# Kernel optimization log

Hardware: AMD Instinct MI355X
Metric: run time of the kernel (lower is better)

The kernel has to match this reference:

```python
import jax, jax.numpy as jnp
import numpy as np
from jax import lax

NMS_THRESH = 0.5
BN_EPS = 1e-5
TO_REMOVE = 1.0  # neural-motifs box convention (+1 in width/height)


def nms_overlaps(boxes):
    # boxes: [N, C, 4] xyxy -> per-class pairwise IoU [N, N, C]
    x1 = jnp.maximum(boxes[:, None, :, 0], boxes[None, :, :, 0])
    y1 = jnp.maximum(boxes[:, None, :, 1], boxes[None, :, :, 1])
    x2 = jnp.minimum(boxes[:, None, :, 2], boxes[None, :, :, 2])
    y2 = jnp.minimum(boxes[:, None, :, 3], boxes[None, :, :, 3])
    inter = jnp.clip(x2 - x1 + TO_REMOVE, 0.0) * jnp.clip(y2 - y1 + TO_REMOVE, 0.0)
    area = (boxes[:, :, 2] - boxes[:, :, 0] + TO_REMOVE) * (boxes[:, :, 3] - boxes[:, :, 1] + TO_REMOVE)  # [N,C]
    union = area[:, None, :] + area[None, :, :] - inter
    return inter / union


def greedy_nms_labels(obj_dists, is_overlap):
    # faithful port of nms_per_cls: iterative argmax + per-class suppression
    N, C = obj_dists.shape
    scores = jax.nn.softmax(obj_dists, axis=-1)
    scores = scores.at[:, 0].set(-1.0)  # kill background column

    def step(carry, _):
        scores, labels = carry
        flat = jnp.argmax(scores)          # row-major, same as np.unravel_index
        box_ind = flat // C
        cls_ind = flat % C
        labels = labels.at[box_ind].set(cls_ind.astype(jnp.int32))
        ov = is_overlap[box_ind, :, cls_ind]  # [N] bool
        col = jnp.where(ov, 0.0, scores[:, cls_ind])
        scores = scores.at[:, cls_ind].set(col)
        scores = scores.at[box_ind, :].set(-1.0)
        return (scores, labels), None

    (_, labels), _ = lax.scan(step, (scores, jnp.zeros(N, jnp.int32)), None, length=N)
    return labels


def setup_inputs() -> dict:
    key = jax.random.key(0)
    ks = jax.random.split(key, 16)
    N, C, D, E, H, P = 400, 151, 4096, 200, 512, 128
    x = jax.random.normal(ks[0], (N, D), jnp.float32)
    predict_logits = jax.random.normal(ks[1], (N, C), jnp.float32) * 2.0
    pos_input = jax.random.uniform(ks[2], (N, 9), jnp.float32)
    xy = jax.random.uniform(ks[3], (N, C, 2), jnp.float32) * 800.0
    wh = jax.random.uniform(ks[4], (N, C, 2), jnp.float32) * 200.0 + 1.0
    boxes_per_cls = jnp.concatenate([xy, xy + wh], axis=-1)
    sc = lambda k, sh: jax.random.normal(k, sh, jnp.float32) * np.float32(1.0 / np.sqrt(sh[0]))
    return {
        'x': x,
        'predict_logits': predict_logits,
        'pos_input': pos_input,
        'boxes_per_cls': boxes_per_cls,
        'obj_embed_w': jax.random.normal(ks[5], (C, E), jnp.float32) * 0.1,
        'obj_embed2_w': jax.random.normal(ks[6], (C, E), jnp.float32) * 0.1,
        'w_pos1': sc(ks[7], (9, 32)), 'b_pos1': jnp.zeros(32, jnp.float32),
        'bn_gamma': jnp.ones(32, jnp.float32), 'bn_beta': jnp.zeros(32, jnp.float32),
        'bn_mean': jnp.zeros(32, jnp.float32), 'bn_var': jnp.ones(32, jnp.float32),
        'w_pos2': sc(ks[8], (32, P)), 'b_pos2': jnp.zeros(P, jnp.float32),
        'w_lin': sc(ks[9], (D + E + P, H)), 'b_lin': jnp.zeros(H, jnp.float32),
        'w_out': sc(ks[10], (H, C)), 'b_out': jnp.zeros(C, jnp.float32),
        'w_fc': sc(ks[11], (D + E + P, H)), 'b_fc': jnp.zeros(H, jnp.float32),
    }


def reference(x, predict_logits, pos_input, boxes_per_cls, obj_embed_w, obj_embed2_w,
              w_pos1, b_pos1, bn_gamma, bn_beta, bn_mean, bn_var, w_pos2, b_pos2,
              w_lin, b_lin, w_out, b_out, w_fc, b_fc):
    # sgdet inference path of VTransEFeaturePE.forward
    obj_embed = jax.nn.softmax(predict_logits, axis=-1) @ obj_embed_w           # [N,E]
    h = pos_input @ w_pos1 + b_pos1                                             # Linear(9,32)
    h = (h - bn_mean) / jnp.sqrt(bn_var + BN_EPS) * bn_gamma + bn_beta          # BN eval
    pos_embed = jax.nn.relu(h @ w_pos2 + b_pos2)                                # [N,128]
    rep = jnp.concatenate([x, obj_embed, pos_embed], axis=-1)                   # [N,4424]
    obj_dists = (rep @ w_lin + b_lin) @ w_out + b_out                           # [N,C]
    is_overlap = nms_overlaps(boxes_per_cls) >= NMS_THRESH                      # [N,N,C]
    obj_preds = greedy_nms_labels(obj_dists, is_overlap)                        # [N] int32
    obj_embed2 = obj_embed2_w[obj_preds]                                        # [N,E]
    obj_rel_rep = jnp.concatenate([x, pos_embed, obj_embed2], axis=-1)
    edge_ctx = jax.nn.relu(obj_rel_rep @ w_fc + b_fc)                           # [N,H]
    return (obj_dists, obj_preds, edge_ctx)
```

## Files before the change

### kernel.cpp

```cpp
#include <hip/hip_runtime.h>
#include <hip/hip_bf16.h>
#include <stdint.h>

#define NB 400
#define NC 151
#define DX 4096
#define DE 200
#define DP 128
#define DH 512
#define KREP 4424
#define TAILW 328
#define MPAD 416
#define SPLITK 8
#define TILES1 139
#define TILES2 132
#define SKSTRIDE 152

__device__ __forceinline__ uint32_t f2ord(float f) {
  uint32_t u = __float_as_uint(f);
  return (u & 0x80000000u) ? ~u : (u | 0x80000000u);
}

__global__ __launch_bounds__(256) void k_embed(
    const float* __restrict__ logits, const float* __restrict__ obj_embed_w,
    const float* __restrict__ pos_input, const float* __restrict__ w_pos1,
    const float* __restrict__ b_pos1, const float* __restrict__ bn_gamma,
    const float* __restrict__ bn_beta, const float* __restrict__ bn_mean,
    const float* __restrict__ bn_var, const float* __restrict__ w_pos2,
    const float* __restrict__ b_pos2, float* __restrict__ tail1) {
  int r = blockIdx.x, t = threadIdx.x;
  if (r >= NB) {
    if (t < TAILW) tail1[r * TAILW + t] = 0.f;
    return;
  }
  __shared__ float p[NC];
  __shared__ float red[256];
  __shared__ float hb[32];

  float v = (t < NC) ? logits[r * NC + t] : -INFINITY;
  red[t] = v; __syncthreads();
  for (int s = 128; s > 0; s >>= 1) { if (t < s) red[t] = fmaxf(red[t], red[t + s]); __syncthreads(); }
  float m = red[0]; __syncthreads();
  float e = (t < NC) ? expf(v - m) : 0.f;
  red[t] = e; __syncthreads();
  for (int s = 128; s > 0; s >>= 1) { if (t < s) red[t] += red[t + s]; __syncthreads(); }
  float sum = red[0];
  if (t < NC) p[t] = e / sum;

  if (t < 32) {
    float acc = b_pos1[t];
    for (int k = 0; k < 9; k++) acc += pos_input[r * 9 + k] * w_pos1[k * 32 + t];
    acc = (acc - bn_mean[t]) / sqrtf(bn_var[t] + 1e-5f) * bn_gamma[t] + bn_beta[t];
    hb[t] = acc;
  }
  __syncthreads();

  if (t < DE) {
    float acc = 0.f;
    for (int k = 0; k < NC; k++) acc += p[k] * obj_embed_w[k * DE + t];
    tail1[r * TAILW + t] = acc;
  }
  if (t < DP) {
    float acc = b_pos2[t];
    for (int k = 0; k < 32; k++) acc += hb[k] * w_pos2[k * DP + t];
    tail1[r * TAILW + DE + t] = fmaxf(acc, 0.f);
  }
}

__device__ __forceinline__ void gemm_body(
    float (*As)[36], float (*Bs)[68],
    const float* __restrict__ x, const float* __restrict__ tail,
    const float* __restrict__ w, float* __restrict__ part,
    int bid, int tiles, int toff) {
  int tid = threadIdx.x;
  int n0 = (bid & 7) * 64, m0 = ((bid >> 3) % 13) * 32;
  int z = bid / 104;
  int tbeg = (z * tiles) / SPLITK, tend = ((z + 1) * tiles) / SPLITK;
  int ty = tid >> 4, tx = tid & 15;
  int a_r = tid >> 3, a_c = (tid & 7) << 2;
  int b_r = tid >> 4, b_c = (tid & 15) << 2;
  float4 acc0 = {0, 0, 0, 0}, acc1 = {0, 0, 0, 0};

  auto loadA = [&](int t) -> float4 {
    int k = t * 32 + a_c;
    int row = m0 + a_r;
    float4 v = {0, 0, 0, 0};
    if (k < KREP) {
      if (k < DX) { if (row < NB) v = *(const float4*)&x[(size_t)row * DX + k]; }
      else v = *(const float4*)&tail[row * TAILW + toff + (k - DX)];
    }
    return v;
  };
  auto loadB = [&](int t, int roff) -> float4 {
    int k = t * 32 + b_r + roff;
    float4 v = {0, 0, 0, 0};
    if (k < KREP) v = *(const float4*)&w[(size_t)k * DH + n0 + b_c];
    return v;
  };

  float4 pa = loadA(tbeg), pb0 = loadB(tbeg, 0), pb1 = loadB(tbeg, 16);
  for (int t = tbeg; t < tend; t++) {
    __syncthreads();
    *(float4*)&As[a_r][a_c] = pa;
    *(float4*)&Bs[b_r][b_c] = pb0;
    *(float4*)&Bs[b_r + 16][b_c] = pb1;
    __syncthreads();
    if (t + 1 < tend) { pa = loadA(t + 1); pb0 = loadB(t + 1, 0); pb1 = loadB(t + 1, 16); }
#pragma unroll
    for (int k4 = 0; k4 < 8; k4++) {
      float4 a0 = *(float4*)&As[ty * 2][k4 * 4];
      float4 a1 = *(float4*)&As[ty * 2 + 1][k4 * 4];
#pragma unroll
      for (int j = 0; j < 4; j++) {
        float4 bv = *(float4*)&Bs[k4 * 4 + j][tx * 4];
        float av0 = (&a0.x)[j], av1 = (&a1.x)[j];
        acc0.x += av0 * bv.x; acc0.y += av0 * bv.y; acc0.z += av0 * bv.z; acc0.w += av0 * bv.w;
        acc1.x += av1 * bv.x; acc1.y += av1 * bv.y; acc1.z += av1 * bv.z; acc1.w += av1 * bv.w;
      }
    }
  }
  int row0 = m0 + ty * 2, col = n0 + tx * 4;
  float* base = part + (size_t)z * NB * DH;
  if (row0 < NB)     *(float4*)&base[row0 * DH + col] = acc0;
  if (row0 + 1 < NB) *(float4*)&base[(row0 + 1) * DH + col] = acc1;
}

__global__ __launch_bounds__(256) void k_g1ov(
    const float* __restrict__ x, const float* __restrict__ tail1,
    const float* __restrict__ w_lin, float* __restrict__ part,
    const float* __restrict__ boxes, uint64_t* __restrict__ ov_bits) {
  __shared__ __align__(16) float As[32][36];
  __shared__ __align__(16) float Bs[32][68];
  int bid = blockIdx.x;
  if (bid >= 832) {
    int c = bid - 832;
    int t = threadIdx.x;
    __shared__ float4 bx[NB];
    const float4* bp4 = (const float4*)boxes;
    for (int j = t; j < NB; j += 256) bx[j] = bp4[j * NC + c];
    __syncthreads();
    int wave = t >> 6, lane = t & 63;
    for (int b = wave; b < NB; b += 4) {
      float4 A = bx[b];
      float areaA = (A.z - A.x + 1.f) * (A.w - A.y + 1.f);
      for (int chunk = 0; chunk < 7; chunk++) {
        int j = chunk * 64 + lane;
        bool ov = false;
        if (j < NB) {
          float4 B = bx[j];
          float x1 = fmaxf(A.x, B.x), y1 = fmaxf(A.y, B.y);
          float x2 = fminf(A.z, B.z), y2 = fminf(A.w, B.w);
          float iw = fmaxf(x2 - x1 + 1.f, 0.f), ih = fmaxf(y2 - y1 + 1.f, 0.f);
          float inter = iw * ih;
          float areaB = (B.z - B.x + 1.f) * (B.w - B.y + 1.f);
          ov = (inter / (areaA + areaB - inter)) >= 0.5f;
        }
        uint64_t mask = __ballot(ov);
        if (lane == 0) ov_bits[((size_t)(b * NC + c) << 3) + chunk] = mask;
      }
    }
    return;
  }
  gemm_body(As, Bs, x, tail1, w_lin, part, bid, TILES1, 0);
}

__global__ __launch_bounds__(256) void k_dists(
    const float* __restrict__ part, const float* __restrict__ b_lin,
    const float* __restrict__ w_out, const float* __restrict__ b_out,
    float* __restrict__ out_dists, uint64_t* __restrict__ skeys) {
  int r = blockIdx.x, t = threadIdx.x;
  __shared__ float h[DH];
  __shared__ float red[256];
  __shared__ float sval[NC];
  float s0 = b_lin[t], s1 = b_lin[t + 256];
#pragma unroll
  for (int z = 0; z < SPLITK; z++) {
    const float* pr = part + ((size_t)z * NB + r) * DH;
    s0 += pr[t]; s1 += pr[t + 256];
  }
  h[t] = s0; h[t + 256] = s1;
  __syncthreads();

  float acc = -INFINITY;
  if (t < NC) {
    acc = b_out[t];
    for (int k = 0; k < DH; k++) acc += h[k] * w_out[k * NC + t];
    out_dists[r * NC + t] = acc;
  }
  red[t] = (t < NC) ? acc : -INFINITY; __syncthreads();
  for (int s = 128; s > 0; s >>= 1) { if (t < s) red[t] = fmaxf(red[t], red[t + s]); __syncthreads(); }
  float mx = red[0]; __syncthreads();
  float e = (t < NC) ? expf(acc - mx) : 0.f;
  red[t] = e; __syncthreads();
  for (int s = 128; s > 0; s >>= 1) { if (t < s) red[t] += red[t + s]; __syncthreads(); }
  float sum = red[0];
  if (t < NC) sval[t] = e / sum;
  __syncthreads();

  if (t >= 1 && t < NC) {
    float v = sval[t];
    int rank = 0;
    for (int c2 = 1; c2 < NC; c2++) {
      float v2 = sval[c2];
      rank += (v2 > v) || (v2 == v && c2 < t);
    }
    skeys[(size_t)r * SKSTRIDE + rank] =
        ((uint64_t)f2ord(v) << 17) | ((uint64_t)(511 - r) << 8) | (uint64_t)t;
  }
}

struct GemmSm { float As[32][36]; float Bs[32][68]; };
struct NmsSm  { uint64_t top4[4][4]; uint64_t ovw[4][8]; int nap; };

__global__ __launch_bounds__(256) void k_nms_g2a(
    const uint64_t* __restrict__ ov_bits, const uint64_t* __restrict__ skeys,
    int* __restrict__ labels_g, float* __restrict__ out_preds,
    const float* __restrict__ x, const float* __restrict__ tail1,
    const float* __restrict__ w_fc, float* __restrict__ part) {
  __shared__ __align__(16) union { GemmSm g; NmsSm n; } sm;
  if (blockIdx.x > 0) {
    gemm_body(sm.g.As, sm.g.Bs, x, tail1, w_fc, part, blockIdx.x - 1, TILES2, DE);
    return;
  }
  int tid = threadIdx.x, wave = tid >> 6, lane = tid & 63;
  int S0w = wave * 2;
  uint64_t cand[2];
  uint64_t supp0[2], supp1[2], supp2[2];
  int depth[2];
  bool removed[2];
  int reszmin[2];

#pragma unroll
  for (int u = 0; u < 2; u++) {
    int r = (S0w + u) * 64 + lane;
    supp0[u] = supp1[u] = supp2[u] = 0;
    depth[u] = 0; removed[u] = false; reszmin[u] = 255;
    if (r < NB) {
      cand[u] = skeys[(size_t)r * SKSTRIDE];
      labels_g[r] = 0; out_preds[r] = 0.f;
    } else cand[u] = 0;
  }

  auto cswap = [](uint64_t& a, uint64_t& b) {
    uint64_t hi = a > b ? a : b, lo = a > b ? b : a; a = hi; b = lo;
  };
  auto merge4 = [&](uint64_t a0, uint64_t a1, uint64_t a2, uint64_t a3,
                    uint64_t e0, uint64_t e1, uint64_t e2, uint64_t e3,
                    uint64_t& o0, uint64_t& o1, uint64_t& o2, uint64_t& o3) {
    uint64_t m0 = a0 > e3 ? a0 : e3;
    uint64_t m1 = a1 > e2 ? a1 : e2;
    uint64_t m2 = a2 > e1 ? a2 : e1;
    uint64_t m3 = a3 > e0 ? a3 : e0;
    cswap(m0, m2); cswap(m1, m3); cswap(m0, m1); cswap(m2, m3);
    o0 = m0; o1 = m1; o2 = m2; o3 = m3;
  };

  int picked = 0;
  while (picked < NB) {
    uint64_t k0 = cand[0] > cand[1] ? cand[0] : cand[1];
    uint64_t k1 = cand[0] > cand[1] ? cand[1] : cand[0];
    uint64_t k2 = 0, k3 = 0;
#pragma unroll
    for (int off = 1; off < 64; off <<= 1) {
      uint64_t p0 = (uint64_t)__shfl_xor((unsigned long long)k0, off, 64);
      uint64_t p1 = (uint64_t)__shfl_xor((unsigned long long)k1, off, 64);
      uint64_t p2 = (uint64_t)__shfl_xor((unsigned long long)k2, off, 64);
      uint64_t p3 = (uint64_t)__shfl_xor((unsigned long long)k3, off, 64);
      uint64_t t0 = k0 > p3 ? k0 : p3;
      uint64_t t1 = k1 > p2 ? k1 : p2;
      uint64_t t2 = k2 > p1 ? k2 : p1;
      uint64_t t3 = k3 > p0 ? k3 : p0;
      cswap(t0, t2); cswap(t1, t3); cswap(t0, t1); cswap(t2, t3);
      k0 = t0; k1 = t1; k2 = t2; k3 = t3;
    }
    if (lane < 4) {
      uint64_t kv = (lane == 0) ? k0 : (lane == 1) ? k1 : (lane == 2) ? k2 : k3;
      sm.n.top4[wave][lane] = kv;
    }
    __syncthreads();

    uint64_t A0 = sm.n.top4[0][0], A1 = sm.n.top4[0][1], A2 = sm.n.top4[0][2], A3 = sm.n.top4[0][3];
    uint64_t B0 = sm.n.top4[1][0], B1 = sm.n.top4[1][1], B2 = sm.n.top4[1][2], B3 = sm.n.top4[1][3];
    uint64_t C0 = sm.n.top4[2][0], C1 = sm.n.top4[2][1], C2 = sm.n.top4[2][2], C3 = sm.n.top4[2][3];
    uint64_t D0 = sm.n.top4[3][0], D1 = sm.n.top4[3][1], D2 = sm.n.top4[3][2], D3 = sm.n.top4[3][3];
    uint64_t P0, P1, P2, P3, Q0, Q1, Q2, Q3, g0, g1, g2, g3;
    merge4(A0, A1, A2, A3, B0, B1, B2, B3, P0, P1, P2, P3);
    merge4(C0, C1, C2, C3, D0, D1, D2, D3, Q0, Q1, Q2, Q3);
    merge4(P0, P1, P2, P3, Q0, Q1, Q2, Q3, g0, g1, g2, g3);

    int b0 = 511 - (int)((g0 >> 8) & 0x1FF), c0 = (int)(g0 & 0xFF);
    int b1 = 511 - (int)((g1 >> 8) & 0x1FF), c1 = (int)(g1 & 0xFF);
    int b2 = 511 - (int)((g2 >> 8) & 0x1FF), c2 = (int)(g2 & 0xFF);
    int b3 = 511 - (int)((g3 >> 8) & 0x1FF), c3 = (int)(g3 & 0xFF);
    int npick = NB - picked; if (npick > 4) npick = 4;

    if (wave == 0) {
      int pi = lane >> 3, pw = lane & 7;
      uint64_t wv = 0;
      if (pi < npick && pw < 7) {
        int bb = (pi == 0) ? b0 : (pi == 1) ? b1 : (pi == 2) ? b2 : b3;
        int cc = (pi == 0) ? c0 : (pi == 1) ? c1 : (pi == 2) ? c2 : c3;
        wv = ov_bits[(((size_t)(bb * NC + cc)) << 3) + pw];
      }
      auto ovb = [&](int ii, int bj) -> bool {
        bool f = ((lane >> 3) == ii) && ((lane & 7) == (bj >> 6)) && ((wv >> (bj & 63)) & 1);
        return __ballot(f) != 0ull;
      };
      uint32_t v1 = (uint32_t)(g1 >> 17), v2 = (uint32_t)(g2 >> 17), v3 = (uint32_t)(g3 >> 17);
      int napl = 1;
      if (npick >= 2 && v1 > 0x80000000u && !(c1 == c0 && ovb(0, b1))) {
        napl = 2;
        if (npick >= 3 && v2 > 0x80000000u &&
            !(c2 == c0 && ovb(0, b2)) && !(c2 == c1 && ovb(1, b2))) {
          napl = 3;
          if (npick >= 4 && v3 > 0x80000000u &&
              !(c3 == c0 && ovb(0, b3)) && !(c3 == c1 && ovb(1, b3)) &&
              !(c3 == c2 && ovb(2, b3)))
            napl = 4;
        }
      }
      if (lane < 32) sm.n.ovw[pi][pw] = wv;
      if (lane == 0) sm.n.nap = napl;
    }
    __syncthreads();
    int napply = sm.n.nap;

#pragma unroll
    for (int u = 0; u < 2; u++) {
      int S = S0w + u;
      int r = S * 64 + lane;
#pragma unroll
      for (int i = 0; i < 4; i++) {
        if (i < napply) {
          int b = (i == 0) ? b0 : (i == 1) ? b1 : (i == 2) ? b2 : b3;
          int c = (i == 0) ? c0 : (i == 1) ? c1 : (i == 2) ? c2 : c3;
          uint64_t owv = sm.n.ovw[i][S];
          if (r == b) {
            removed[u] = true; reszmin[u] = 255;
            cand[u] = ((uint64_t)0x407FFFFFu << 17) | ((uint64_t)(511 - r) << 8);
            labels_g[b] = c; out_preds[b] = (float)c;
          } else if ((owv >> lane) & 1) {
            if (removed[u]) {
              if (c < reszmin[u]) reszmin[u] = c;
              cand[u] = ((uint64_t)0x80000000u << 17) | ((uint64_t)(511 - r) << 8)
                        | (uint64_t)reszmin[u];
            } else {
              uint64_t bit = 1ull << (c & 63);
              if (c < 64) supp0[u] |= bit; else if (c < 128) supp1[u] |= bit; else supp2[u] |= bit;
              if ((int)(cand[u] & 0xFF) == c) {
                int d = depth[u] + 1;
                uint64_t k = 0;
                for (; d < 150; d++) {
                  k = skeys[(size_t)r * SKSTRIDE + d];
                  int col = (int)(k & 0xFF);
                  uint64_t mm = (col < 64) ? supp0[u] : ((col < 128) ? supp1[u] : supp2[u]);
                  if (!((mm >> (col & 63)) & 1)) break;
                }
                if (d >= 150)
                  k = ((uint64_t)0x80000000u << 17) | ((uint64_t)(511 - r) << 8) | 1ull;
                depth[u] = d; cand[u] = k;
              }
            }
          }
        }
      }
    }
    picked += napply;
  }
}

__global__ __launch_bounds__(256) void k_final(
    const float* __restrict__ emb2, const int* __restrict__ labels,
    const float* __restrict__ w_fc, const float* __restrict__ part,
    const float* __restrict__ b_fc, float* __restrict__ out_edge) {
  __shared__ __align__(16) float As[32][36];
  __shared__ __align__(16) float Bs[32][68];
  int tid = threadIdx.x;
  int n0 = blockIdx.x * 64, m0 = blockIdx.y * 32;
  int ty = tid >> 4, tx = tid & 15;
  int a_r = tid >> 3, a_c = (tid & 7) << 2;
  int b_r = tid >> 4, b_c = (tid & 15) << 2;
  float4 acc0 = {0, 0, 0, 0}, acc1 = {0, 0, 0, 0};
  int row_a = m0 + a_r;
  int lab = (row_a < NB) ? labels[row_a] : 0;

  auto loadA = [&](int t) -> float4 {
    int kk = t * 32 + a_c;
    float4 v = {0, 0, 0, 0};
    if (kk < DE && row_a < NB) v = *(const float4*)&emb2[(size_t)lab * DE + kk];
    return v;
  };
  auto loadB = [&](int t, int roff) -> float4 {
    int kk = t * 32 + b_r + roff;
    float4 v = {0, 0, 0, 0};
    if (kk < DE) v = *(const float4*)&w_fc[(size_t)(DX + DP + kk) * DH + n0 + b_c];
    return v;
  };

  float4 pa = loadA(0), pb0 = loadB(0, 0), pb1 = loadB(0, 16);
  for (int t = 0; t < 7; t++) {
    __syncthreads();
    *(float4*)&As[a_r][a_c] = pa;
    *(float4*)&Bs[b_r][b_c] = pb0;
    *(float4*)&Bs[b_r + 16][b_c] = pb1;
    __syncthreads();
    if (t + 1 < 7) { pa = loadA(t + 1); pb0 = loadB(t + 1, 0); pb1 = loadB(t + 1, 16); }
#pragma unroll
    for (int k4 = 0; k4 < 8; k4++) {
      float4 a0 = *(float4*)&As[ty * 2][k4 * 4];
      float4 a1 = *(float4*)&As[ty * 2 + 1][k4 * 4];
#pragma unroll
      for (int j = 0; j < 4; j++) {
        float4 bv = *(float4*)&Bs[k4 * 4 + j][tx * 4];
        float av0 = (&a0.x)[j], av1 = (&a1.x)[j];
        acc0.x += av0 * bv.x; acc0.y += av0 * bv.y; acc0.z += av0 * bv.z; acc0.w += av0 * bv.w;
        acc1.x += av1 * bv.x; acc1.y += av1 * bv.y; acc1.z += av1 * bv.z; acc1.w += av1 * bv.w;
      }
    }
  }
  int row0 = m0 + ty * 2, col = n0 + tx * 4;
#pragma unroll
  for (int z = 0; z < SPLITK; z++) {
    if (row0 < NB) {
      float4 p = *(const float4*)&part[((size_t)z * NB + row0) * DH + col];
      acc0.x += p.x; acc0.y += p.y; acc0.z += p.z; acc0.w += p.w;
    }
    if (row0 + 1 < NB) {
      float4 p = *(const float4*)&part[((size_t)z * NB + row0 + 1) * DH + col];
      acc1.x += p.x; acc1.y += p.y; acc1.z += p.z; acc1.w += p.w;
    }
  }
  float4 bv = *(const float4*)&b_fc[col];
  if (row0 < NB) {
    float4 r;
    r.x = fmaxf(acc0.x + bv.x, 0.f); r.y = fmaxf(acc0.y + bv.y, 0.f);
    r.z = fmaxf(acc0.z + bv.z, 0.f); r.w = fmaxf(acc0.w + bv.w, 0.f);
    *(float4*)&out_edge[row0 * DH + col] = r;
  }
  if (row0 + 1 < NB) {
    float4 r;
    r.x = fmaxf(acc1.x + bv.x, 0.f); r.y = fmaxf(acc1.y + bv.y, 0.f);
    r.z = fmaxf(acc1.z + bv.z, 0.f); r.w = fmaxf(acc1.w + bv.w, 0.f);
    *(float4*)&out_edge[(row0 + 1) * DH + col] = r;
  }
}

extern "C" void kernel_launch(void* const* d_in, const int* in_sizes, int n_in,
                              void* d_out, int out_size, void* d_ws, size_t ws_size,
                              hipStream_t stream) {
  const float* x            = (const float*)d_in[0];
  const float* logits       = (const float*)d_in[1];
  const float* pos_input    = (const float*)d_in[2];
  const float* boxes        = (const float*)d_in[3];
  const float* obj_embed_w  = (const float*)d_in[4];
  const float* obj_embed2_w = (const float*)d_in[5];
  const float* w_pos1       = (const float*)d_in[6];
  const float* b_pos1       = (const float*)d_in[7];
  const float* bn_gamma     = (const float*)d_in[8];
  const float* bn_beta      = (const float*)d_in[9];
  const float* bn_mean      = (const float*)d_in[10];
  const float* bn_var       = (const float*)d_in[11];
  const float* w_pos2       = (const float*)d_in[12];
  const float* b_pos2       = (const float*)d_in[13];
  const float* w_lin        = (const float*)d_in[14];
  const float* b_lin        = (const float*)d_in[15];
  const float* w_out        = (const float*)d_in[16];
  const float* b_out        = (const float*)d_in[17];
  const float* w_fc         = (const float*)d_in[18];
  const float* b_fc         = (const float*)d_in[19];

  float* ws         = (float*)d_ws;
  float* tail1      = ws;
  int* labels       = (int*)(tail1 + MPAD * TAILW);
  uint64_t* skeys   = (uint64_t*)(labels + MPAD);
  uint64_t* ov_bits = skeys + (size_t)NB * SKSTRIDE;
  float* part       = (float*)(ov_bits + (size_t)NB * NC * 8);

  float* out       = (float*)d_out;
  float* out_dists = out;
  float* out_preds = out + NB * NC;
  float* out_edge  = out + NB * NC + NB;

  k_embed<<<MPAD, 256, 0, stream>>>(logits, obj_embed_w, pos_input, w_pos1, b_pos1,
                                    bn_gamma, bn_beta, bn_mean, bn_var, w_pos2, b_pos2,
                                    tail1);
  k_g1ov<<<983, 256, 0, stream>>>(x, tail1, w_lin, part, boxes, ov_bits);
  k_dists<<<NB, 256, 0, stream>>>(part, b_lin, w_out, b_out, out_dists, skeys);
  k_nms_g2a<<<833, 256, 0, stream>>>(ov_bits, skeys, labels, out_preds,
                                     x, tail1, w_fc, part);
  k_final<<<dim3(8, 13), 256, 0, stream>>>(obj_embed2_w, labels, w_fc, part,
                                           b_fc, out_edge);
}
```

Before: 595.8 us.

## Batch up to eight NMS picks per round with redundant per-wave decisions

The greedy NMS loop now merges the per-wave top-4 lists into a global top-8 and applies up to eight non-conflicting picks per round instead of four. Each round's overlap decision is computed redundantly in every wave using ballots, and results are broadcast with shuffles. This removes the second block barrier and the shared-memory broadcast of overlap words, and it double-buffers the top-4 staging array so one barrier per round is enough. Candidates are bounded by each wave's fourth-best key (mincnt) to keep correctness. In exchange every wave performs the overlap-bit loads, and there is more ballot and sorting-network work per round.

```diff
diff --git a/kernel.cpp b/kernel.cpp
--- a/kernel.cpp
+++ b/kernel.cpp
@@ -210,7 +210,7 @@
 }
 
 struct GemmSm { float As[32][36]; float Bs[32][68]; };
-struct NmsSm  { uint64_t top4[4][4]; uint64_t ovw[4][8]; int nap; };
+struct NmsSm  { uint64_t top4[2][4][4]; };
 
 __global__ __launch_bounds__(256) void k_nms_g2a(
     const uint64_t* __restrict__ ov_bits, const uint64_t* __restrict__ skeys,
@@ -244,19 +244,10 @@
   auto cswap = [](uint64_t& a, uint64_t& b) {
     uint64_t hi = a > b ? a : b, lo = a > b ? b : a; a = hi; b = lo;
   };
-  auto merge4 = [&](uint64_t a0, uint64_t a1, uint64_t a2, uint64_t a3,
-                    uint64_t e0, uint64_t e1, uint64_t e2, uint64_t e3,
-                    uint64_t& o0, uint64_t& o1, uint64_t& o2, uint64_t& o3) {
-    uint64_t m0 = a0 > e3 ? a0 : e3;
-    uint64_t m1 = a1 > e2 ? a1 : e2;
-    uint64_t m2 = a2 > e1 ? a2 : e1;
-    uint64_t m3 = a3 > e0 ? a3 : e0;
-    cswap(m0, m2); cswap(m1, m3); cswap(m0, m1); cswap(m2, m3);
-    o0 = m0; o1 = m1; o2 = m2; o3 = m3;
-  };
-
-  int picked = 0;
+
+  int picked = 0, rr = 0;
   while (picked < NB) {
+    int pp = rr & 1; rr++;
     uint64_t k0 = cand[0] > cand[1] ? cand[0] : cand[1];
     uint64_t k1 = cand[0] > cand[1] ? cand[1] : cand[0];
     uint64_t k2 = 0, k3 = 0;
@@ -275,91 +266,119 @@
     }
     if (lane < 4) {
       uint64_t kv = (lane == 0) ? k0 : (lane == 1) ? k1 : (lane == 2) ? k2 : k3;
-      sm.n.top4[wave][lane] = kv;
+      sm.n.top4[pp][wave][lane] = kv;
     }
     __syncthreads();
 
-    uint64_t A0 = sm.n.top4[0][0], A1 = sm.n.top4[0][1], A2 = sm.n.top4[0][2], A3 = sm.n.top4[0][3];
-    uint64_t B0 = sm.n.top4[1][0], B1 = sm.n.top4[1][1], B2 = sm.n.top4[1][2], B3 = sm.n.top4[1][3];
-    uint64_t C0 = sm.n.top4[2][0], C1 = sm.n.top4[2][1], C2 = sm.n.top4[2][2], C3 = sm.n.top4[2][3];
-    uint64_t D0 = sm.n.top4[3][0], D1 = sm.n.top4[3][1], D2 = sm.n.top4[3][2], D3 = sm.n.top4[3][3];
-    uint64_t P0, P1, P2, P3, Q0, Q1, Q2, Q3, g0, g1, g2, g3;
-    merge4(A0, A1, A2, A3, B0, B1, B2, B3, P0, P1, P2, P3);
-    merge4(C0, C1, C2, C3, D0, D1, D2, D3, Q0, Q1, Q2, Q3);
-    merge4(P0, P1, P2, P3, Q0, Q1, Q2, Q3, g0, g1, g2, g3);
-
-    int b0 = 511 - (int)((g0 >> 8) & 0x1FF), c0 = (int)(g0 & 0xFF);
-    int b1 = 511 - (int)((g1 >> 8) & 0x1FF), c1 = (int)(g1 & 0xFF);
-    int b2 = 511 - (int)((g2 >> 8) & 0x1FF), c2 = (int)(g2 & 0xFF);
-    int b3 = 511 - (int)((g3 >> 8) & 0x1FF), c3 = (int)(g3 & 0xFF);
-    int npick = NB - picked; if (npick > 4) npick = 4;
-
-    if (wave == 0) {
-      int pi = lane >> 3, pw = lane & 7;
-      uint64_t wv = 0;
-      if (pi < npick && pw < 7) {
-        int bb = (pi == 0) ? b0 : (pi == 1) ? b1 : (pi == 2) ? b2 : b3;
-        int cc = (pi == 0) ? c0 : (pi == 1) ? c1 : (pi == 2) ? c2 : c3;
-        wv = ov_bits[(((size_t)(bb * NC + cc)) << 3) + pw];
+    uint64_t A0 = sm.n.top4[pp][0][0], A1 = sm.n.top4[pp][0][1], A2 = sm.n.top4[pp][0][2], A3 = sm.n.top4[pp][0][3];
+    uint64_t B0 = sm.n.top4[pp][1][0], B1 = sm.n.top4[pp][1][1], B2 = sm.n.top4[pp][1][2], B3 = sm.n.top4[pp][1][3];
+    uint64_t C0 = sm.n.top4[pp][2][0], C1 = sm.n.top4[pp][2][1], C2 = sm.n.top4[pp][2][2], C3 = sm.n.top4[pp][2][3];
+    uint64_t D0 = sm.n.top4[pp][3][0], D1 = sm.n.top4[pp][3][1], D2 = sm.n.top4[pp][3][2], D3 = sm.n.top4[pp][3][3];
+    uint64_t x0 = A0, x1 = A1, x2 = A2, x3 = A3, x4 = B3, x5 = B2, x6 = B1, x7 = B0;
+    cswap(x0,x4); cswap(x1,x5); cswap(x2,x6); cswap(x3,x7);
+    cswap(x0,x2); cswap(x1,x3); cswap(x4,x6); cswap(x5,x7);
+    cswap(x0,x1); cswap(x2,x3); cswap(x4,x5); cswap(x6,x7);
+    uint64_t y0 = C0, y1 = C1, y2 = C2, y3 = C3, y4 = D3, y5 = D2, y6 = D1, y7 = D0;
+    cswap(y0,y4); cswap(y1,y5); cswap(y2,y6); cswap(y3,y7);
+    cswap(y0,y2); cswap(y1,y3); cswap(y4,y6); cswap(y5,y7);
+    cswap(y0,y1); cswap(y2,y3); cswap(y4,y5); cswap(y6,y7);
+    uint64_t tk[8];
+    tk[0] = x0 > y7 ? x0 : y7;  tk[1] = x1 > y6 ? x1 : y6;
+    tk[2] = x2 > y5 ? x2 : y5;  tk[3] = x3 > y4 ? x3 : y4;
+    tk[4] = x4 > y3 ? x4 : y3;  tk[5] = x5 > y2 ? x5 : y2;
+    tk[6] = x6 > y1 ? x6 : y1;  tk[7] = x7 > y0 ? x7 : y0;
+    cswap(tk[0],tk[4]); cswap(tk[1],tk[5]); cswap(tk[2],tk[6]); cswap(tk[3],tk[7]);
+    cswap(tk[0],tk[2]); cswap(tk[1],tk[3]); cswap(tk[4],tk[6]); cswap(tk[5],tk[7]);
+    cswap(tk[0],tk[1]); cswap(tk[2],tk[3]); cswap(tk[4],tk[5]); cswap(tk[6],tk[7]);
+
+    int cntA = 0, cntB = 0, cntC = 0, cntD = 0;
+#pragma unroll
+    for (int i = 0; i < 8; i++) {
+      cntA += (tk[i] > A3); cntB += (tk[i] > B3);
+      cntC += (tk[i] > C3); cntD += (tk[i] > D3);
+    }
+    int mincnt = cntA < cntB ? cntA : cntB;
+    mincnt = mincnt < cntC ? mincnt : cntC;
+    mincnt = mincnt < cntD ? mincnt : cntD;
+
+    int npick = NB - picked; if (npick > 8) npick = 8;
+
+    int pi = lane >> 3, pw = lane & 7;
+    int bsel = 0, csel = 0;
+#pragma unroll
+    for (int i = 0; i < 8; i++)
+      if (pi == i) {
+        bsel = 511 - (int)((tk[i] >> 8) & 0x1FF);
+        csel = (int)(tk[i] & 0xFF);
       }
-      auto ovb = [&](int ii, int bj) -> bool {
-        bool f = ((lane >> 3) == ii) && ((lane & 7) == (bj >> 6)) && ((wv >> (bj & 63)) & 1);
-        return __ballot(f) != 0ull;
-      };
-      uint32_t v1 = (uint32_t)(g1 >> 17), v2 = (uint32_t)(g2 >> 17), v3 = (uint32_t)(g3 >> 17);
-      int napl = 1;
-      if (npick >= 2 && v1 > 0x80000000u && !(c1 == c0 && ovb(0, b1))) {
-        napl = 2;
-        if (npick >= 3 && v2 > 0x80000000u &&
-            !(c2 == c0 && ovb(0, b2)) && !(c2 == c1 && ovb(1, b2))) {
-          napl = 3;
-          if (npick >= 4 && v3 > 0x80000000u &&
-              !(c3 == c0 && ovb(0, b3)) && !(c3 == c1 && ovb(1, b3)) &&
-              !(c3 == c2 && ovb(2, b3)))
-            napl = 4;
-        }
-      }
-      if (lane < 32) sm.n.ovw[pi][pw] = wv;
-      if (lane == 0) sm.n.nap = napl;
-    }
-    __syncthreads();
-    int napply = sm.n.nap;
+    uint64_t wv = 0;
+    if (pi < npick && pw < 7)
+      wv = ov_bits[(((size_t)(bsel * NC + csel)) << 3) + pw];
+    uint32_t packed = ((uint32_t)bsel << 8) | (uint32_t)csel;
+
+    uint64_t balnz_raw = __ballot(wv != 0ull);
+
+    uint64_t ovall = 0;
+#pragma unroll
+    for (int j = 0; j < 8; j++) {
+      int bj = 511 - (int)((tk[j] >> 8) & 0x1FF);
+      bool hit = (pw == (bj >> 6)) && ((wv >> (bj & 63)) & 1);
+      uint64_t bal = __ballot(hit);
+      bal |= bal >> 4; bal |= bal >> 2; bal |= bal >> 1;
+      uint32_t m8 = (uint32_t)(((bal & 0x0101010101010101ULL) * 0x0102040810204080ULL) >> 56);
+      ovall |= (uint64_t)m8 << (8 * j);
+    }
+
+    int napply = 1; bool stop = false;
+#pragma unroll
+    for (int j = 1; j < 8; j++) {
+      bool bad = (j >= npick) || (j > mincnt) ||
+                 ((uint32_t)(tk[j] >> 17) <= 0x80000000u);
+      int cjv = (int)(tk[j] & 0xFF);
+#pragma unroll
+      for (int i = 0; i < j; i++)
+        bad = bad || (((int)(tk[i] & 0xFF) == cjv) && ((ovall >> (8 * j + i)) & 1));
+      stop = stop || bad;
+      if (!stop) napply = j + 1;
+    }
+
+    uint64_t am = (napply >= 8) ? ~0ull : ((1ull << (8 * napply)) - 1);
+    uint64_t balnz = balnz_raw & am;
 
 #pragma unroll
     for (int u = 0; u < 2; u++) {
       int S = S0w + u;
       int r = S * 64 + lane;
-#pragma unroll
-      for (int i = 0; i < 4; i++) {
-        if (i < napply) {
-          int b = (i == 0) ? b0 : (i == 1) ? b1 : (i == 2) ? b2 : b3;
-          int c = (i == 0) ? c0 : (i == 1) ? c1 : (i == 2) ? c2 : c3;
-          uint64_t owv = sm.n.ovw[i][S];
-          if (r == b) {
-            removed[u] = true; reszmin[u] = 255;
-            cand[u] = ((uint64_t)0x407FFFFFu << 17) | ((uint64_t)(511 - r) << 8);
-            labels_g[b] = c; out_preds[b] = (float)c;
-          } else if ((owv >> lane) & 1) {
-            if (removed[u]) {
-              if (c < reszmin[u]) reszmin[u] = c;
-              cand[u] = ((uint64_t)0x80000000u << 17) | ((uint64_t)(511 - r) << 8)
-                        | (uint64_t)reszmin[u];
-            } else {
-              uint64_t bit = 1ull << (c & 63);
-              if (c < 64) supp0[u] |= bit; else if (c < 128) supp1[u] |= bit; else supp2[u] |= bit;
-              if ((int)(cand[u] & 0xFF) == c) {
-                int d = depth[u] + 1;
-                uint64_t k = 0;
-                for (; d < 150; d++) {
-                  k = skeys[(size_t)r * SKSTRIDE + d];
-                  int col = (int)(k & 0xFF);
-                  uint64_t mm = (col < 64) ? supp0[u] : ((col < 128) ? supp1[u] : supp2[u]);
-                  if (!((mm >> (col & 63)) & 1)) break;
-                }
-                if (d >= 150)
-                  k = ((uint64_t)0x80000000u << 17) | ((uint64_t)(511 - r) << 8) | 1ull;
-                depth[u] = d; cand[u] = k;
+      for (int i = 0; i < napply; i++) {
+        int bc = __shfl((int)packed, i * 8, 64);
+        int b = (bc >> 8) & 0x1FF, c = bc & 0xFF;
+        bool act = ((balnz >> (i * 8 + S)) & 1) || ((b >> 6) == S);
+        if (!act) continue;
+        uint64_t owv = (uint64_t)__shfl((unsigned long long)wv, i * 8 + S, 64);
+        if (r == b) {
+          removed[u] = true; reszmin[u] = 255;
+          cand[u] = ((uint64_t)0x407FFFFFu << 17) | ((uint64_t)(511 - r) << 8);
+          labels_g[b] = c; out_preds[b] = (float)c;
+        } else if ((owv >> lane) & 1) {
+          if (removed[u]) {
+            if (c < reszmin[u]) reszmin[u] = c;
+            cand[u] = ((uint64_t)0x80000000u << 17) | ((uint64_t)(511 - r) << 8)
+                      | (uint64_t)reszmin[u];
+          } else {
+            uint64_t bit = 1ull << (c & 63);
+            if (c < 64) supp0[u] |= bit; else if (c < 128) supp1[u] |= bit; else supp2[u] |= bit;
+            if ((int)(cand[u] & 0xFF) == c) {
+              int d = depth[u] + 1;
+              uint64_t k = 0;
+              for (; d < 150; d++) {
+                k = skeys[(size_t)r * SKSTRIDE + d];
+                int col = (int)(k & 0xFF);
+                uint64_t mm = (col < 64) ? supp0[u] : ((col < 128) ? supp1[u] : supp2[u]);
+                if (!((mm >> (col & 63)) & 1)) break;
               }
+              if (d >= 150)
+                k = ((uint64_t)0x80000000u << 17) | ((uint64_t)(511 - r) << 8) | 1ull;
+              depth[u] = d; cand[u] = k;
             }
           }
         }
```

Result: no change. 585.2 us (-1.8%).
